# Kernel optimization log

Measured on AMD Instinct MI355X. Metric: run time of the kernel, lower is better.

## Reference

```python
import jax, jax.numpy as jnp
import numpy as np

B, C, N, H = 4, 512, 16384, 8
D = C // H
EPS = 1e-6

def setup_inputs() -> dict:
    key = jax.random.key(0)
    k1, k2, k3 = jax.random.split(key, 3)
    # xavier_normal std for Linear(C, out): sqrt(2/(fan_in+fan_out))
    std_qkv = (2.0 / (C + 3 * C)) ** 0.5
    std_proj = (2.0 / (C + C)) ** 0.5
    return {
        "x": jax.random.normal(k1, (B, C, N), dtype=jnp.float32),
        "W_qkv": jax.random.normal(k2, (C, 3 * C), dtype=jnp.float32) * std_qkv,
        "b_qkv": jnp.zeros((3 * C,), dtype=jnp.float32),
        "W_proj": jax.random.normal(k3, (C, C), dtype=jnp.float32) * std_proj,
        "b_proj": jnp.zeros((C,), dtype=jnp.float32),
    }

def _phi(x):
    return jax.nn.elu(x) + 1.0

def reference(x, W_qkv, b_qkv, W_proj, b_proj):
    # x: [B, C, N] -> [B, N, C]
    xt = jnp.swapaxes(x, 1, 2)
    qkv = xt @ W_qkv + b_qkv                      # [B, N, 3C]
    q, k, v = jnp.split(qkv, 3, axis=-1)
    # [B, N, C] -> [B, H, N, D]
    def heads(t):
        return jnp.swapaxes(t.reshape(B, N, H, D), 1, 2)
    q, k, v = heads(q), heads(k), heads(v)
    q_phi = _phi(q)                               # [B, H, N, D]
    k_phi = _phi(k)
    S = jnp.einsum('bhnd,bhne->bhde', k_phi, v)   # [B, H, D, D] KV state
    k_sum = k_phi.sum(axis=-2)                    # [B, H, D]
    num = jnp.einsum('bhnd,bhde->bhne', q_phi, S) # [B, H, N, D]
    den = jnp.einsum('bhnd,bhd->bhn', q_phi, k_sum)[..., None] + EPS
    out = num / den                               # [B, H, N, D]
    out = jnp.swapaxes(out, 1, 2).reshape(B, N, C)
    out = out @ W_proj + b_proj                   # [B, N, C]
    return jnp.swapaxes(out, 1, 2)                # [B, C, N]
```

## Files before the change

### kernel.cpp

```cpp
#include <hip/hip_runtime.h>
#include <cmath>

#define B_  4
#define C_  512
#define N_  16384
#define H_  8
#define D_  64
#define C3_ 1536
#define EPS 1e-6f

#define PADA 72
#define PADT 136
#define PADO 132

typedef __attribute__((ext_vector_type(8))) short bf16x8;
typedef __attribute__((ext_vector_type(4))) float f32x4;

__device__ __forceinline__ ushort f2bf(float f) {
    union { float f; unsigned u; } c{f};
    unsigned r = (c.u + 0x7FFF + ((c.u >> 16) & 1)) >> 16;
    return (ushort)r;
}
__device__ __forceinline__ float bf2f(ushort b) {
    union { unsigned u; float f; } c{(unsigned)b << 16};
    return c.f;
}
__device__ __forceinline__ float phi_f(float x) { return x > 0.f ? x + 1.f : __expf(x); }

__global__ __launch_bounds__(256) void k_transpose(
        const float* __restrict__ src, ushort* __restrict__ dst,
        int R, int Cc, long sStride, long dStride) {
    __shared__ ushort T[64][72];
    const long sb = (long)blockIdx.z * sStride;
    const long db = (long)blockIdx.z * dStride;
    const int c0 = blockIdx.x * 64, r0 = blockIdx.y * 64;
    const int t = threadIdx.x;
    const int ct = t & 15, rt = t >> 4;
    float4 v[4];
    #pragma unroll
    for (int k = 0; k < 4; ++k)
        v[k] = *(const float4*)(src + sb + (long)(r0 + rt * 4 + k) * Cc + c0 + ct * 4);
    #pragma unroll
    for (int j = 0; j < 4; ++j) {
        ushort pk[4];
        #pragma unroll
        for (int k = 0; k < 4; ++k) pk[k] = f2bf(((const float*)&v[k])[j]);
        *(uint2*)&T[ct * 4 + j][rt * 4] = *(uint2*)pk;
    }
    __syncthreads();
    const int c = t >> 2, rq = (t & 3) * 16;
    ushort* d = dst + db + (long)(c0 + c) * R + r0 + rq;
    *(int4*)(d)     = *(const int4*)&T[c][rq];
    *(int4*)(d + 8) = *(const int4*)&T[c][rq + 8];
}

__global__ __launch_bounds__(256) void k_kv_s(
        const ushort* __restrict__ xt, const ushort* __restrict__ Wqt,
        const float* __restrict__ bqkv, float* __restrict__ S_g,
        float* __restrict__ ksum_g) {
    const int s = blockIdx.x, h = blockIdx.y, b = blockIdx.z;
    const int tid = threadIdx.x;
    const int w = tid >> 6, ln = tid & 63, lr = ln & 15, lq = ln >> 4;
    const int bh = b * H_ + h;

    __shared__ __align__(16) char smem[128 * PADA * 2 * 2];
    ushort (*Ax)[PADA]  = (ushort(*)[PADA])smem;
    ushort (*Bw)[PADA]  = (ushort(*)[PADA])(smem + 128 * PADA * 2);
    ushort (*kvT)[PADT] = (ushort(*)[PADT])smem;
    __shared__ float biasL[128];
    __shared__ float ksRed[4][64];

    if (tid < 128) {
        int col = tid < 64 ? (512 + h * 64 + tid) : (1024 + h * 64 + (tid - 64));
        biasL[tid] = bqkv[col];
    }

    const f32x4 FZ = {0.f, 0.f, 0.f, 0.f};
    f32x4 Sacc[4] = {FZ, FZ, FZ, FZ};
    float ksp = 0.f;

    for (int it = 0; it < 8; ++it) {
        const int n0 = (s * 8 + it) * 128;
        f32x4 acc[2][8];
        #pragma unroll
        for (int mi = 0; mi < 2; mi++)
            #pragma unroll
            for (int ji = 0; ji < 8; ji++) acc[mi][ji] = FZ;

        for (int kc = 0; kc < 8; ++kc) {
            const int c0 = kc * 64;
            __syncthreads();
            {
                int row = tid >> 1, co = (tid & 1) * 32;
                const int4* srca = (const int4*)(xt + ((long)(b * N_ + n0 + row)) * C_ + c0 + co);
                int4* dsta = (int4*)&Ax[row][co];
                dsta[0] = srca[0]; dsta[1] = srca[1]; dsta[2] = srca[2]; dsta[3] = srca[3];
                int j = row;
                int wr = j < 64 ? (512 + h * 64 + j) : (1024 + h * 64 + (j - 64));
                const int4* srcb = (const int4*)(Wqt + (long)wr * C_ + c0 + co);
                int4* dstb = (int4*)&Bw[j][co];
                dstb[0] = srcb[0]; dstb[1] = srcb[1]; dstb[2] = srcb[2]; dstb[3] = srcb[3];
            }
            __syncthreads();
            #pragma unroll
            for (int ks = 0; ks < 2; ++ks) {
                bf16x8 a[2], bb[8];
                #pragma unroll
                for (int mi = 0; mi < 2; mi++)
                    a[mi] = *(const bf16x8*)&Ax[w * 32 + mi * 16 + lr][ks * 32 + lq * 8];
                #pragma unroll
                for (int ji = 0; ji < 8; ji++)
                    bb[ji] = *(const bf16x8*)&Bw[ji * 16 + lr][ks * 32 + lq * 8];
                #pragma unroll
                for (int mi = 0; mi < 2; mi++)
                    #pragma unroll
                    for (int ji = 0; ji < 8; ji++)
                        acc[mi][ji] = __builtin_amdgcn_mfma_f32_16x16x32_bf16(
                            a[mi], bb[ji], acc[mi][ji], 0, 0, 0);
            }
        }
        __syncthreads();
        #pragma unroll
        for (int mi = 0; mi < 2; mi++) {
            int nl = w * 32 + mi * 16 + lq * 4;
            #pragma unroll
            for (int ji = 0; ji < 8; ji++) {
                int j = ji * 16 + lr;
                float bs = biasL[j];
                ushort pk[4];
                #pragma unroll
                for (int r = 0; r < 4; r++) {
                    float vv = acc[mi][ji][r] + bs;
                    if (j < 64) vv = phi_f(vv);
                    pk[r] = f2bf(vv);
                }
                *(uint2*)&kvT[j][nl] = *(uint2*)pk;
            }
        }
        __syncthreads();
        #pragma unroll
        for (int ks = 0; ks < 4; ++ks) {
            bf16x8 af = *(const bf16x8*)&kvT[w * 16 + lr][ks * 32 + lq * 8];
            #pragma unroll
            for (int e = 0; e < 4; e++) {
                bf16x8 bv = *(const bf16x8*)&kvT[64 + e * 16 + lr][ks * 32 + lq * 8];
                Sacc[e] = __builtin_amdgcn_mfma_f32_16x16x32_bf16(af, bv, Sacc[e], 0, 0, 0);
            }
        }
        {
            int d = tid & 63, q = tid >> 6;
            float sum = 0.f;
            #pragma unroll
            for (int m = 0; m < 4; m++) {
                bf16x8 u = *(const bf16x8*)&kvT[d][q * 32 + m * 8];
                #pragma unroll
                for (int j = 0; j < 8; j++) sum += bf2f((ushort)u[j]);
            }
            ksp += sum;
        }
    }
    #pragma unroll
    for (int e = 0; e < 4; e++)
        #pragma unroll
        for (int r = 0; r < 4; r++)
            atomicAdd(&S_g[((long)bh * 64 + w * 16 + lq * 4 + r) * 64 + e * 16 + lr],
                      Sacc[e][r]);
    ksRed[tid >> 6][tid & 63] = ksp;
    __syncthreads();
    if (tid < 64)
        atomicAdd(&ksum_g[bh * 64 + tid],
                  ksRed[0][tid] + ksRed[1][tid] + ksRed[2][tid] + ksRed[3][tid]);
}

__global__ void k_sfin(const float* __restrict__ S_g, const float* __restrict__ ksum_g,
                       ushort* __restrict__ SbT) {
    int bh = blockIdx.x, t = threadIdx.x;
    for (int i = t; i < 5120; i += 256) {
        int e = i >> 6, d = i & 63;
        float v = (e < 64) ? S_g[(long)bh * 4096 + d * 64 + e]
                           : (e == 64 ? ksum_g[bh * 64 + d] : 0.f);
        ushort hi = f2bf(v);
        ushort lo = f2bf(v - bf2f(hi));
        SbT[(long)bh * 10240 + i] = hi;
        SbT[(long)bh * 10240 + 5120 + i] = lo;
    }
}

__global__ __launch_bounds__(256) void k_q_attn(
        const ushort* __restrict__ xt, const ushort* __restrict__ Wqt,
        const float* __restrict__ bqkv, const ushort* __restrict__ SbT,
        ushort* __restrict__ attn) {
    const int nt = blockIdx.x, h = blockIdx.y, b = blockIdx.z;
    const int n0 = nt * 128;
    const int tid = threadIdx.x;
    const int w = tid >> 6, ln = tid & 63, lr = ln & 15, lq = ln >> 4;
    const int bh = b * H_ + h;

    __shared__ __align__(16) ushort Ax[128][PADA];
    __shared__ __align__(16) ushort Bq[64][PADA];
    __shared__ __align__(16) ushort Sb[160][PADA];
    __shared__ float denL[128];

    #pragma unroll
    for (int p = 0; p < 5; ++p) {
        int r = p * 32 + (tid >> 3);
        *(int4*)&Sb[r][(tid & 7) * 8] =
            *(const int4*)(SbT + (long)bh * 10240 + r * 64 + (tid & 7) * 8);
    }

    const f32x4 FZ = {0.f, 0.f, 0.f, 0.f};
    f32x4 accq[2][4];
    #pragma unroll
    for (int mi = 0; mi < 2; mi++)
        #pragma unroll
        for (int ji = 0; ji < 4; ji++) accq[mi][ji] = FZ;

    for (int kc = 0; kc < 8; ++kc) {
        const int c0 = kc * 64;
        __syncthreads();
        {
            int row = tid >> 1, co = (tid & 1) * 32;
            const int4* srca = (const int4*)(xt + ((long)(b * N_ + n0 + row)) * C_ + c0 + co);
            int4* dsta = (int4*)&Ax[row][co];
            dsta[0] = srca[0]; dsta[1] = srca[1]; dsta[2] = srca[2]; dsta[3] = srca[3];
            if (tid < 128) {
                int j = tid >> 1;
                const int4* srcb = (const int4*)(Wqt + (long)(h * 64 + j) * C_ + c0 + co);
                int4* dstb = (int4*)&Bq[j][co];
                dstb[0] = srcb[0]; dstb[1] = srcb[1]; dstb[2] = srcb[2]; dstb[3] = srcb[3];
            }
        }
        __syncthreads();
        #pragma unroll
        for (int ks = 0; ks < 2; ++ks) {
            bf16x8 a[2], bb[4];
            #pragma unroll
            for (int mi = 0; mi < 2; mi++)
                a[mi] = *(const bf16x8*)&Ax[w * 32 + mi * 16 + lr][ks * 32 + lq * 8];
            #pragma unroll
            for (int ji = 0; ji < 4; ji++)
                bb[ji] = *(const bf16x8*)&Bq[ji * 16 + lr][ks * 32 + lq * 8];
            #pragma unroll
            for (int mi = 0; mi < 2; mi++)
                #pragma unroll
                for (int ji = 0; ji < 4; ji++)
                    accq[mi][ji] = __builtin_amdgcn_mfma_f32_16x16x32_bf16(
                        a[mi], bb[ji], accq[mi][ji], 0, 0, 0);
        }
    }
    __syncthreads();
    #pragma unroll
    for (int mi = 0; mi < 2; mi++) {
        int nl = w * 32 + mi * 16 + lq * 4;
        #pragma unroll
        for (int ji = 0; ji < 4; ji++) {
            int d = ji * 16 + lr;
            float bs = bqkv[h * 64 + d];
            #pragma unroll
            for (int r = 0; r < 4; r++)
                Ax[nl + r][d] = f2bf(phi_f(accq[mi][ji][r] + bs));
        }
    }
    __syncthreads();
    f32x4 accn[2][5];
    #pragma unroll
    for (int mi = 0; mi < 2; mi++)
        #pragma unroll
        for (int ei = 0; ei < 5; ei++) accn[mi][ei] = FZ;
    #pragma unroll
    for (int ks = 0; ks < 2; ++ks) {
        bf16x8 a[2];
        #pragma unroll
        for (int mi = 0; mi < 2; mi++)
            a[mi] = *(const bf16x8*)&Ax[w * 32 + mi * 16 + lr][ks * 32 + lq * 8];
        #pragma unroll
        for (int ei = 0; ei < 5; ei++) {
            bf16x8 bhi = *(const bf16x8*)&Sb[ei * 16 + lr][ks * 32 + lq * 8];
            bf16x8 blo = *(const bf16x8*)&Sb[80 + ei * 16 + lr][ks * 32 + lq * 8];
            #pragma unroll
            for (int mi = 0; mi < 2; mi++) {
                accn[mi][ei] = __builtin_amdgcn_mfma_f32_16x16x32_bf16(
                    a[mi], bhi, accn[mi][ei], 0, 0, 0);
                accn[mi][ei] = __builtin_amdgcn_mfma_f32_16x16x32_bf16(
                    a[mi], blo, accn[mi][ei], 0, 0, 0);
            }
        }
    }
    if (lr == 0) {
        #pragma unroll
        for (int mi = 0; mi < 2; mi++)
            #pragma unroll
            for (int r = 0; r < 4; r++)
                denL[w * 32 + mi * 16 + lq * 4 + r] = accn[mi][4][r] + EPS;
    }
    __syncthreads();
    #pragma unroll
    for (int mi = 0; mi < 2; mi++) {
        int nl = w * 32 + mi * 16 + lq * 4;
        #pragma unroll
        for (int ji = 0; ji < 4; ji++) {
            int e = ji * 16 + lr;
            #pragma unroll
            for (int r = 0; r < 4; r++)
                Ax[nl + r][e] = f2bf(accn[mi][ji][r] / denL[nl + r]);
        }
    }
    __syncthreads();
    {
        int row = tid >> 1, co = (tid & 1) * 32;
        const int4* sp = (const int4*)&Ax[row][co];
        int4* dp = (int4*)(attn + ((long)(b * N_ + n0 + row)) * C_ + h * 64 + co);
        dp[0] = sp[0]; dp[1] = sp[1]; dp[2] = sp[2]; dp[3] = sp[3];
    }
}

__global__ __launch_bounds__(256) void k_proj(
        const ushort* __restrict__ attn, const ushort* __restrict__ Wpt,
        const float* __restrict__ bproj, float* __restrict__ out) {
    const int nt = blockIdx.x, jt = blockIdx.y;
    const int tid = threadIdx.x;
    const int w = tid >> 6, ln = tid & 63, lr = ln & 15, lq = ln >> 4;
    const int b = nt >> 7;
    const int nloc = (nt & 127) * 128;

    __shared__ __align__(16) char smem[128 * PADA * 2 * 2];
    ushort (*Aa)[PADA] = (ushort(*)[PADA])smem;
    ushort (*Bw)[PADA] = (ushort(*)[PADA])(smem + 128 * PADA * 2);
    float (*outT)[PADO] = (float(*)[PADO])smem;

    const f32x4 FZ = {0.f, 0.f, 0.f, 0.f};
    f32x4 acc[2][8];
    #pragma unroll
    for (int mi = 0; mi < 2; mi++)
        #pragma unroll
        for (int ji = 0; ji < 8; ji++) acc[mi][ji] = FZ;

    for (int kc = 0; kc < 8; ++kc) {
        const int c0 = kc * 64;
        __syncthreads();
        {
            int row = tid >> 1, co = (tid & 1) * 32;
            const int4* srca = (const int4*)(attn + ((long)(nt * 128 + row)) * C_ + c0 + co);
            int4* dsta = (int4*)&Aa[row][co];
            dsta[0] = srca[0]; dsta[1] = srca[1]; dsta[2] = srca[2]; dsta[3] = srca[3];
            int j = row;
            const int4* srcb = (const int4*)(Wpt + (long)(jt * 128 + j) * C_ + c0 + co);
            int4* dstb = (int4*)&Bw[j][co];
            dstb[0] = srcb[0]; dstb[1] = srcb[1]; dstb[2] = srcb[2]; dstb[3] = srcb[3];
        }
        __syncthreads();
        #pragma unroll
        for (int ks = 0; ks < 2; ++ks) {
            bf16x8 a[2], bb[8];
            #pragma unroll
            for (int mi = 0; mi < 2; mi++)
                a[mi] = *(const bf16x8*)&Aa[w * 32 + mi * 16 + lr][ks * 32 + lq * 8];
            #pragma unroll
            for (int ji = 0; ji < 8; ji++)
                bb[ji] = *(const bf16x8*)&Bw[ji * 16 + lr][ks * 32 + lq * 8];
            #pragma unroll
            for (int mi = 0; mi < 2; mi++)
                #pragma unroll
                for (int ji = 0; ji < 8; ji++)
                    acc[mi][ji] = __builtin_amdgcn_mfma_f32_16x16x32_bf16(
                        a[mi], bb[ji], acc[mi][ji], 0, 0, 0);
        }
    }
    #pragma unroll
    for (int half = 0; half < 2; ++half) {
        __syncthreads();
        #pragma unroll
        for (int mi = 0; mi < 2; mi++) {
            int nl = w * 32 + mi * 16 + lq * 4;
            #pragma unroll
            for (int ji = 0; ji < 4; ji++) {
                int cl = ji * 16 + lr;
                float bs = bproj[jt * 128 + half * 64 + cl];
                f32x4 v = acc[mi][half * 4 + ji];
                #pragma unroll
                for (int r = 0; r < 4; r++) v[r] += bs;
                *(f32x4*)&outT[cl][nl] = v;
            }
        }
        __syncthreads();
        {
            int cl = tid >> 2, ch = (tid & 3) * 32;
            const float* sp = &outT[cl][ch];
            float* dp = out + ((long)(b * C_ + jt * 128 + half * 64 + cl)) * N_ + nloc + ch;
            #pragma unroll
            for (int k = 0; k < 8; ++k)
                ((float4*)dp)[k] = ((const float4*)sp)[k];
        }
    }
}

__global__ __launch_bounds__(256) void kernelA_fb(
        const float* __restrict__ x, const float* __restrict__ Wqkv,
        const float* __restrict__ bqkv, float* __restrict__ S_g,
        float* __restrict__ ksum_g) {
    const int h = blockIdx.x;
    const int s = blockIdx.y;
    const int b = blockIdx.z;
    const int tid = threadIdx.x;
    const int tn = tid & 15;
    const int tj = tid >> 4;
    const int td = tid & 15;
    const int te = tid >> 4;

    __shared__ float As[16][64];
    __shared__ float Bs[16][128];
    __shared__ float kphi_s[64][64];
    __shared__ float v_s[64][64];

    float acc2[4][4];
    #pragma unroll
    for (int i = 0; i < 4; i++)
        #pragma unroll
        for (int j = 0; j < 4; j++) acc2[i][j] = 0.f;
    float ksum_r = 0.f;

    float bias_j[8];
    #pragma unroll
    for (int jj = 0; jj < 8; jj++) {
        int j = tj * 8 + jj;
        int col = (j < 64) ? (512 + h * 64 + j) : (1024 + h * 64 + (j - 64));
        bias_j[jj] = bqkv[col];
    }

    for (int it = 0; it < 8; ++it) {
        const int n0 = (s * 8 + it) * 64;
        float acc[4][8];
        #pragma unroll
        for (int i = 0; i < 4; i++)
            #pragma unroll
            for (int jj = 0; jj < 8; jj++) acc[i][jj] = 0.f;

        for (int kc = 0; kc < 32; ++kc) {
            const int c0 = kc * 16;
            __syncthreads();
            {
                int r = tid >> 4, n4 = (tid & 15) * 4;
                const float* src = x + ((size_t)b * C_ + (c0 + r)) * (size_t)N_ + n0 + n4;
                *(float4*)&As[r][n4] = *(const float4*)src;
            }
            #pragma unroll
            for (int part = 0; part < 2; ++part) {
                int idx = tid + part * 256;
                int r = idx >> 5;
                int j4 = (idx & 31) * 4;
                int col = (j4 < 64) ? (512 + h * 64 + j4) : (1024 + h * 64 + (j4 - 64));
                const float* src = Wqkv + (size_t)(c0 + r) * C3_ + col;
                *(float4*)&Bs[r][j4] = *(const float4*)src;
            }
            __syncthreads();
            #pragma unroll
            for (int k = 0; k < 16; ++k) {
                float a[4], bb[8];
                *(float4*)a      = *(const float4*)&As[k][tn * 4];
                *(float4*)&bb[0] = *(const float4*)&Bs[k][tj * 8];
                *(float4*)&bb[4] = *(const float4*)&Bs[k][tj * 8 + 4];
                #pragma unroll
                for (int i = 0; i < 4; i++)
                    #pragma unroll
                    for (int jj = 0; jj < 8; jj++)
                        acc[i][jj] = fmaf(a[i], bb[jj], acc[i][jj]);
            }
        }
        __syncthreads();
        if (tj < 8) {
            #pragma unroll
            for (int i = 0; i < 4; i++) {
                int n = tn * 4 + i;
                float tmp[8];
                #pragma unroll
                for (int jj = 0; jj < 8; jj++) tmp[jj] = phi_f(acc[i][jj] + bias_j[jj]);
                *(float4*)&kphi_s[n][tj * 8]     = *(float4*)&tmp[0];
                *(float4*)&kphi_s[n][tj * 8 + 4] = *(float4*)&tmp[4];
            }
        } else {
            #pragma unroll
            for (int i = 0; i < 4; i++) {
                int n = tn * 4 + i;
                float tmp[8];
                #pragma unroll
                for (int jj = 0; jj < 8; jj++) tmp[jj] = acc[i][jj] + bias_j[jj];
                *(float4*)&v_s[n][(tj - 8) * 8]     = *(float4*)&tmp[0];
                *(float4*)&v_s[n][(tj - 8) * 8 + 4] = *(float4*)&tmp[4];
            }
        }
        __syncthreads();
        #pragma unroll 4
        for (int n = 0; n < 64; ++n) {
            float a[4], bb[4];
            *(float4*)a  = *(const float4*)&kphi_s[n][td * 4];
            *(float4*)bb = *(const float4*)&v_s[n][te * 4];
            #pragma unroll
            for (int dd = 0; dd < 4; dd++)
                #pragma unroll
                for (int ee = 0; ee < 4; ee++)
                    acc2[dd][ee] = fmaf(a[dd], bb[ee], acc2[dd][ee]);
        }
        if (tid < 64) {
            float sum = 0.f;
            #pragma unroll 8
            for (int n = 0; n < 64; ++n) sum += kphi_s[n][tid];
            ksum_r += sum;
        }
    }

    const int bh = b * H_ + h;
    #pragma unroll
    for (int dd = 0; dd < 4; dd++)
        #pragma unroll
        for (int ee = 0; ee < 4; ee++)
            atomicAdd(&S_g[((size_t)bh * 64 + td * 4 + dd) * 64 + te * 4 + ee], acc2[dd][ee]);
    if (tid < 64) atomicAdd(&ksum_g[bh * 64 + tid], ksum_r);
}

__global__ __launch_bounds__(256) void kernelB_fb(
        const float* __restrict__ x, const float* __restrict__ Wqkv,
        const float* __restrict__ bqkv, const float* __restrict__ Wproj,
        const float* __restrict__ bproj, const float* __restrict__ S_g,
        const float* __restrict__ ksum_g, float* __restrict__ out) {
    const int nt = blockIdx.x;
    const int b  = blockIdx.y;
    const int n0 = nt * 16;
    const int tid = threadIdx.x;
    const int tn = tid & 3;
    const int tj = tid >> 2;

    __shared__ float QA[512][16];
    __shared__ float As[16][16];
    __shared__ float Bs2[16][256];
    __shared__ float SB[16][64];
    __shared__ float ksumL[512];
    __shared__ float denL[16];

    ksumL[tid]       = ksum_g[(size_t)b * 512 + tid];
    ksumL[tid + 256] = ksum_g[(size_t)b * 512 + tid + 256];

    for (int half = 0; half < 2; ++half) {
        float acc[4][4];
        #pragma unroll
        for (int i = 0; i < 4; i++)
            #pragma unroll
            for (int j = 0; j < 4; j++) acc[i][j] = 0.f;

        for (int kc = 0; kc < 32; ++kc) {
            const int c0 = kc * 16;
            __syncthreads();
            {
                int r = tid >> 4, n = tid & 15;
                As[r][n] = x[((size_t)b * C_ + c0 + r) * (size_t)N_ + n0 + n];
            }
            {
                int r = tid >> 4;
                int j0 = (tid & 15) * 16;
                const float* src = Wqkv + (size_t)(c0 + r) * C3_ + half * 256 + j0;
                float4* dst = (float4*)&Bs2[r][j0];
                #pragma unroll
                for (int q4 = 0; q4 < 4; q4++) dst[q4] = ((const float4*)src)[q4];
            }
            __syncthreads();
            #pragma unroll
            for (int k = 0; k < 16; ++k) {
                float a[4], bb[4];
                *(float4*)a  = *(const float4*)&As[k][tn * 4];
                *(float4*)bb = *(const float4*)&Bs2[k][tj * 4];
                #pragma unroll
                for (int i = 0; i < 4; i++)
                    #pragma unroll
                    for (int jj = 0; jj < 4; jj++)
                        acc[i][jj] = fmaf(a[i], bb[jj], acc[i][jj]);
            }
        }
        #pragma unroll
        for (int jj = 0; jj < 4; jj++) {
            int c = half * 256 + tj * 4 + jj;
            float bq = bqkv[c];
            float tmp[4];
            #pragma unroll
            for (int i = 0; i < 4; i++) tmp[i] = phi_f(acc[i][jj] + bq);
            *(float4*)&QA[c][tn * 4] = *(float4*)tmp;
        }
    }
    __syncthreads();

    for (int h = 0; h < H_; ++h) {
        if (tid < 16) {
            float d = 0.f;
            #pragma unroll 8
            for (int dd = 0; dd < 64; ++dd)
                d = fmaf(QA[h * 64 + dd][tid], ksumL[h * 64 + dd], d);
            denL[tid] = d + EPS;
        }
        float acc4[4] = {0.f, 0.f, 0.f, 0.f};
        for (int dc = 0; dc < 4; ++dc) {
            __syncthreads();
            {
                int r = tid >> 4, e4 = (tid & 15) * 4;
                *(float4*)&SB[r][e4] =
                    *(const float4*)&S_g[(((size_t)(b * H_ + h)) * 64 + dc * 16 + r) * 64 + e4];
            }
            __syncthreads();
            #pragma unroll
            for (int k = 0; k < 16; ++k) {
                float a[4];
                *(float4*)a = *(const float4*)&QA[h * 64 + dc * 16 + k][tn * 4];
                float bb = SB[k][tj];
                #pragma unroll
                for (int i = 0; i < 4; i++) acc4[i] = fmaf(a[i], bb, acc4[i]);
            }
        }
        __syncthreads();
        {
            float tmp[4];
            #pragma unroll
            for (int i = 0; i < 4; i++) tmp[i] = acc4[i] / denL[tn * 4 + i];
            *(float4*)&QA[h * 64 + tj][tn * 4] = *(float4*)tmp;
        }
        __syncthreads();
    }

    for (int half = 0; half < 2; ++half) {
        float acc[4][4];
        #pragma unroll
        for (int i = 0; i < 4; i++)
            #pragma unroll
            for (int j = 0; j < 4; j++) acc[i][j] = 0.f;

        for (int kc = 0; kc < 32; ++kc) {
            __syncthreads();
            {
                int r = tid >> 4;
                int j0 = (tid & 15) * 16;
                const float* src = Wproj + (size_t)(kc * 16 + r) * C_ + half * 256 + j0;
                float4* dst = (float4*)&Bs2[r][j0];
                #pragma unroll
                for (int q4 = 0; q4 < 4; q4++) dst[q4] = ((const float4*)src)[q4];
            }
            __syncthreads();
            #pragma unroll
            for (int k = 0; k < 16; ++k) {
                float a[4], bb[4];
                *(float4*)a  = *(const float4*)&QA[kc * 16 + k][tn * 4];
                *(float4*)bb = *(const float4*)&Bs2[k][tj * 4];
                #pragma unroll
                for (int i = 0; i < 4; i++)
                    #pragma unroll
                    for (int jj = 0; jj < 4; jj++)
                        acc[i][jj] = fmaf(a[i], bb[jj], acc[i][jj]);
            }
        }
        #pragma unroll
        for (int jj = 0; jj < 4; jj++) {
            int c = half * 256 + tj * 4 + jj;
            float bp = bproj[c];
            float tmp[4];
            #pragma unroll
            for (int i = 0; i < 4; i++) tmp[i] = acc[i][jj] + bp;
            *(float4*)&out[((size_t)b * C_ + c) * (size_t)N_ + n0 + tn * 4] = *(float4*)tmp;
        }
    }
}

extern "C" void kernel_launch(void* const* d_in, const int* in_sizes, int n_in,
                              void* d_out, int out_size, void* d_ws, size_t ws_size,
                              hipStream_t stream) {
    const float* x     = (const float*)d_in[0];
    const float* Wqkv  = (const float*)d_in[1];
    const float* bqkv  = (const float*)d_in[2];
    const float* Wproj = (const float*)d_in[3];
    const float* bproj = (const float*)d_in[4];
    float* out = (float*)d_out;

    const size_t oS    = 0;
    const size_t oK    = oS + 524288;
    const size_t oXT   = oK + 8192;
    const size_t oWq   = oXT + 67108864;
    const size_t oWp   = oWq + 1572864;
    const size_t oSbT  = oWp + 524288;
    const size_t oAttn = oSbT + 655360;
    const size_t need  = oAttn + 67108864;

    float* S_g    = (float*)((char*)d_ws + oS);
    float* ksum_g = (float*)((char*)d_ws + oK);

    if (ws_size < need) {
        hipMemsetAsync(d_ws, 0, 532480, stream);
        kernelA_fb<<<dim3(H_, 32, B_), 256, 0, stream>>>(x, Wqkv, bqkv, S_g, ksum_g);
        kernelB_fb<<<dim3(N_ / 16, B_), 256, 0, stream>>>(x, Wqkv, bqkv, Wproj, bproj,
                                                          S_g, ksum_g, out);
        return;
    }

    ushort* xt   = (ushort*)((char*)d_ws + oXT);
    ushort* Wqt  = (ushort*)((char*)d_ws + oWq);
    ushort* Wpt  = (ushort*)((char*)d_ws + oWp);
    ushort* SbT  = (ushort*)((char*)d_ws + oSbT);
    ushort* attn = (ushort*)((char*)d_ws + oAttn);

    hipMemsetAsync(d_ws, 0, 532480, stream);
    k_transpose<<<dim3(N_ / 64, C_ / 64, B_), 256, 0, stream>>>(
        x, xt, C_, N_, (long)C_ * N_, (long)N_ * C_);
    k_transpose<<<dim3(C3_ / 64, C_ / 64, 1), 256, 0, stream>>>(
        Wqkv, Wqt, C_, C3_, 0, 0);
    k_transpose<<<dim3(C_ / 64, C_ / 64, 1), 256, 0, stream>>>(
        Wproj, Wpt, C_, C_, 0, 0);
    k_kv_s<<<dim3(16, H_, B_), 256, 0, stream>>>(xt, Wqt, bqkv, S_g, ksum_g);
    k_sfin<<<dim3(B_ * H_), 256, 0, stream>>>(S_g, ksum_g, SbT);
    k_q_attn<<<dim3(N_ / 128, H_, B_), 256, 0, stream>>>(xt, Wqt, bqkv, SbT, attn);
    k_proj<<<dim3((B_ * N_) / 128, 4), 256, 0, stream>>>(attn, Wpt, bproj, out);
}
```

Baseline: 534.4 us.

## Use direct global-to-LDS loads with XOR-swizzled layout in GEMM kernels

Replaces the register-staged global-to-shared copies in the KV-state, Q-attention and projection kernels with global_load_lds 16-byte direct loads into unpadded tiles that use an XOR swizzle to avoid bank conflicts. The k_sum reduction is computed with an MFMA against a ones vector instead of a scalar LDS reduction. The KV kernel grid is doubled with fewer iterations per block to raise parallelism. The cost is more complex swizzled indexing and more atomic traffic from the larger KV grid.

```diff
diff --git a/kernel.cpp b/kernel.cpp
--- a/kernel.cpp
+++ b/kernel.cpp
@@ -15,6 +15,15 @@
 
 typedef __attribute__((ext_vector_type(8))) short bf16x8;
 typedef __attribute__((ext_vector_type(4))) float f32x4;
+
+typedef const void __attribute__((address_space(1)))* gas_t;
+typedef void __attribute__((address_space(3)))* las_t;
+
+__device__ __forceinline__ void gld16(const void* g, void* l) {
+    __builtin_amdgcn_global_load_lds((gas_t)(unsigned long long)g,
+                                     (las_t)(unsigned)(unsigned long long)l,
+                                     16, 0, 0);
+}
 
 __device__ __forceinline__ ushort f2bf(float f) {
     union { float f; unsigned u; } c{f};
@@ -62,25 +71,40 @@
     const int tid = threadIdx.x;
     const int w = tid >> 6, ln = tid & 63, lr = ln & 15, lq = ln >> 4;
     const int bh = b * H_ + h;
-
-    __shared__ __align__(16) char smem[128 * PADA * 2 * 2];
-    ushort (*Ax)[PADA]  = (ushort(*)[PADA])smem;
-    ushort (*Bw)[PADA]  = (ushort(*)[PADA])(smem + 128 * PADA * 2);
+    const int lrow = ln >> 3;
+    const int csw  = (ln & 7) ^ lrow;
+    const int sw   = lr & 7;
+
+    __shared__ __align__(16) char smem[34816];
+    ushort* AxL = (ushort*)smem;
+    ushort* BwL = (ushort*)(smem + 16384);
     ushort (*kvT)[PADT] = (ushort(*)[PADT])smem;
     __shared__ float biasL[128];
-    __shared__ float ksRed[4][64];
 
     if (tid < 128) {
         int col = tid < 64 ? (512 + h * 64 + tid) : (1024 + h * 64 + (tid - 64));
         biasL[tid] = bqkv[col];
     }
 
+    int gA[4], gB[4];
+    #pragma unroll
+    for (int i = 0; i < 4; ++i) {
+        const int row = (w * 4 + i) * 8 + lrow;
+        gA[i] = row * C_ + csw * 8;
+        const int wr = row < 64 ? (512 + h * 64 + row) : (1024 + h * 64 + (row - 64));
+        gB[i] = wr * C_ + csw * 8;
+    }
+    const long xb = (long)b * N_ * C_;
+
     const f32x4 FZ = {0.f, 0.f, 0.f, 0.f};
     f32x4 Sacc[4] = {FZ, FZ, FZ, FZ};
-    float ksp = 0.f;
-
-    for (int it = 0; it < 8; ++it) {
-        const int n0 = (s * 8 + it) * 128;
+    f32x4 Kacc = FZ;
+    bf16x8 ONES;
+    #pragma unroll
+    for (int i = 0; i < 8; ++i) ONES[i] = (short)0x3F80;
+
+    for (int it = 0; it < 4; ++it) {
+        const ushort* xa = xt + xb + (long)((s * 4 + it) * 128) * C_;
         f32x4 acc[2][8];
         #pragma unroll
         for (int mi = 0; mi < 2; mi++)
@@ -90,27 +114,23 @@
         for (int kc = 0; kc < 8; ++kc) {
             const int c0 = kc * 64;
             __syncthreads();
-            {
-                int row = tid >> 1, co = (tid & 1) * 32;
-                const int4* srca = (const int4*)(xt + ((long)(b * N_ + n0 + row)) * C_ + c0 + co);
-                int4* dsta = (int4*)&Ax[row][co];
-                dsta[0] = srca[0]; dsta[1] = srca[1]; dsta[2] = srca[2]; dsta[3] = srca[3];
-                int j = row;
-                int wr = j < 64 ? (512 + h * 64 + j) : (1024 + h * 64 + (j - 64));
-                const int4* srcb = (const int4*)(Wqt + (long)wr * C_ + c0 + co);
-                int4* dstb = (int4*)&Bw[j][co];
-                dstb[0] = srcb[0]; dstb[1] = srcb[1]; dstb[2] = srcb[2]; dstb[3] = srcb[3];
+            #pragma unroll
+            for (int i = 0; i < 4; ++i) {
+                const int ch = w * 4 + i;
+                gld16(xa + gA[i] + c0, AxL + ch * 512);
+                gld16(Wqt + gB[i] + c0, BwL + ch * 512);
             }
             __syncthreads();
             #pragma unroll
             for (int ks = 0; ks < 2; ++ks) {
+                const int cof = ((ks * 4 + lq) ^ sw) * 8;
                 bf16x8 a[2], bb[8];
                 #pragma unroll
                 for (int mi = 0; mi < 2; mi++)
-                    a[mi] = *(const bf16x8*)&Ax[w * 32 + mi * 16 + lr][ks * 32 + lq * 8];
+                    a[mi] = *(const bf16x8*)&AxL[(w * 32 + mi * 16 + lr) * 64 + cof];
                 #pragma unroll
                 for (int ji = 0; ji < 8; ji++)
-                    bb[ji] = *(const bf16x8*)&Bw[ji * 16 + lr][ks * 32 + lq * 8];
+                    bb[ji] = *(const bf16x8*)&BwL[(ji * 16 + lr) * 64 + cof];
                 #pragma unroll
                 for (int mi = 0; mi < 2; mi++)
                     #pragma unroll
@@ -146,17 +166,7 @@
                 bf16x8 bv = *(const bf16x8*)&kvT[64 + e * 16 + lr][ks * 32 + lq * 8];
                 Sacc[e] = __builtin_amdgcn_mfma_f32_16x16x32_bf16(af, bv, Sacc[e], 0, 0, 0);
             }
-        }
-        {
-            int d = tid & 63, q = tid >> 6;
-            float sum = 0.f;
-            #pragma unroll
-            for (int m = 0; m < 4; m++) {
-                bf16x8 u = *(const bf16x8*)&kvT[d][q * 32 + m * 8];
-                #pragma unroll
-                for (int j = 0; j < 8; j++) sum += bf2f((ushort)u[j]);
-            }
-            ksp += sum;
+            Kacc = __builtin_amdgcn_mfma_f32_16x16x32_bf16(af, ONES, Kacc, 0, 0, 0);
         }
     }
     #pragma unroll
@@ -165,11 +175,11 @@
         for (int r = 0; r < 4; r++)
             atomicAdd(&S_g[((long)bh * 64 + w * 16 + lq * 4 + r) * 64 + e * 16 + lr],
                       Sacc[e][r]);
-    ksRed[tid >> 6][tid & 63] = ksp;
-    __syncthreads();
-    if (tid < 64)
-        atomicAdd(&ksum_g[bh * 64 + tid],
-                  ksRed[0][tid] + ksRed[1][tid] + ksRed[2][tid] + ksRed[3][tid]);
+    if (lr == 0) {
+        #pragma unroll
+        for (int r = 0; r < 4; r++)
+            atomicAdd(&ksum_g[bh * 64 + w * 16 + lq * 4 + r], Kacc[r]);
+    }
 }
 
 __global__ void k_sfin(const float* __restrict__ S_g, const float* __restrict__ ksum_g,
@@ -195,9 +205,10 @@
     const int tid = threadIdx.x;
     const int w = tid >> 6, ln = tid & 63, lr = ln & 15, lq = ln >> 4;
     const int bh = b * H_ + h;
-
-    __shared__ __align__(16) ushort Ax[128][PADA];
-    __shared__ __align__(16) ushort Bq[64][PADA];
+    const int lrow = ln >> 3, csw = (ln & 7) ^ lrow, sw = lr & 7;
+
+    __shared__ __align__(16) ushort AxL[128 * 64];
+    __shared__ __align__(16) ushort BqL[64 * 64];
     __shared__ __align__(16) ushort Sb[160][PADA];
     __shared__ float denL[128];
 
@@ -208,6 +219,18 @@
             *(const int4*)(SbT + (long)bh * 10240 + r * 64 + (tid & 7) * 8);
     }
 
+    int gA[4], gB[2];
+    #pragma unroll
+    for (int i = 0; i < 4; ++i) {
+        const int row = (w * 4 + i) * 8 + lrow;
+        gA[i] = (b * N_ + n0 + row) * C_ + csw * 8;
+    }
+    #pragma unroll
+    for (int i = 0; i < 2; ++i) {
+        const int j = (w * 2 + i) * 8 + lrow;
+        gB[i] = (h * 64 + j) * C_ + csw * 8;
+    }
+
     const f32x4 FZ = {0.f, 0.f, 0.f, 0.f};
     f32x4 accq[2][4];
     #pragma unroll
@@ -218,28 +241,23 @@
     for (int kc = 0; kc < 8; ++kc) {
         const int c0 = kc * 64;
         __syncthreads();
-        {
-            int row = tid >> 1, co = (tid & 1) * 32;
-            const int4* srca = (const int4*)(xt + ((long)(b * N_ + n0 + row)) * C_ + c0 + co);
-            int4* dsta = (int4*)&Ax[row][co];
-            dsta[0] = srca[0]; dsta[1] = srca[1]; dsta[2] = srca[2]; dsta[3] = srca[3];
-            if (tid < 128) {
-                int j = tid >> 1;
-                const int4* srcb = (const int4*)(Wqt + (long)(h * 64 + j) * C_ + c0 + co);
-                int4* dstb = (int4*)&Bq[j][co];
-                dstb[0] = srcb[0]; dstb[1] = srcb[1]; dstb[2] = srcb[2]; dstb[3] = srcb[3];
-            }
-        }
+        #pragma unroll
+        for (int i = 0; i < 4; ++i)
+            gld16(xt + gA[i] + c0, AxL + (w * 4 + i) * 512);
+        #pragma unroll
+        for (int i = 0; i < 2; ++i)
+            gld16(Wqt + gB[i] + c0, BqL + (w * 2 + i) * 512);
         __syncthreads();
         #pragma unroll
         for (int ks = 0; ks < 2; ++ks) {
+            const int cof = ((ks * 4 + lq) ^ sw) * 8;
             bf16x8 a[2], bb[4];
             #pragma unroll
             for (int mi = 0; mi < 2; mi++)
-                a[mi] = *(const bf16x8*)&Ax[w * 32 + mi * 16 + lr][ks * 32 + lq * 8];
+                a[mi] = *(const bf16x8*)&AxL[(w * 32 + mi * 16 + lr) * 64 + cof];
             #pragma unroll
             for (int ji = 0; ji < 4; ji++)
-                bb[ji] = *(const bf16x8*)&Bq[ji * 16 + lr][ks * 32 + lq * 8];
+                bb[ji] = *(const bf16x8*)&BqL[(ji * 16 + lr) * 64 + cof];
             #pragma unroll
             for (int mi = 0; mi < 2; mi++)
                 #pragma unroll
@@ -257,8 +275,11 @@
             int d = ji * 16 + lr;
             float bs = bqkv[h * 64 + d];
             #pragma unroll
-            for (int r = 0; r < 4; r++)
-                Ax[nl + r][d] = f2bf(phi_f(accq[mi][ji][r] + bs));
+            for (int r = 0; r < 4; r++) {
+                int row = nl + r;
+                AxL[row * 64 + ((((d >> 3) ^ (row & 7)) << 3) | (d & 7))] =
+                    f2bf(phi_f(accq[mi][ji][r] + bs));
+            }
         }
     }
     __syncthreads();
@@ -269,10 +290,11 @@
         for (int ei = 0; ei < 5; ei++) accn[mi][ei] = FZ;
     #pragma unroll
     for (int ks = 0; ks < 2; ++ks) {
+        const int cof = ((ks * 4 + lq) ^ sw) * 8;
         bf16x8 a[2];
         #pragma unroll
         for (int mi = 0; mi < 2; mi++)
-            a[mi] = *(const bf16x8*)&Ax[w * 32 + mi * 16 + lr][ks * 32 + lq * 8];
+            a[mi] = *(const bf16x8*)&AxL[(w * 32 + mi * 16 + lr) * 64 + cof];
         #pragma unroll
         for (int ei = 0; ei < 5; ei++) {
             bf16x8 bhi = *(const bf16x8*)&Sb[ei * 16 + lr][ks * 32 + lq * 8];
@@ -301,16 +323,20 @@
         for (int ji = 0; ji < 4; ji++) {
             int e = ji * 16 + lr;
             #pragma unroll
-            for (int r = 0; r < 4; r++)
-                Ax[nl + r][e] = f2bf(accn[mi][ji][r] / denL[nl + r]);
+            for (int r = 0; r < 4; r++) {
+                int row = nl + r;
+                AxL[row * 64 + ((((e >> 3) ^ (row & 7)) << 3) | (e & 7))] =
+                    f2bf(accn[mi][ji][r] / denL[row]);
+            }
         }
     }
     __syncthreads();
     {
         int row = tid >> 1, co = (tid & 1) * 32;
-        const int4* sp = (const int4*)&Ax[row][co];
         int4* dp = (int4*)(attn + ((long)(b * N_ + n0 + row)) * C_ + h * 64 + co);
-        dp[0] = sp[0]; dp[1] = sp[1]; dp[2] = sp[2]; dp[3] = sp[3];
+        #pragma unroll
+        for (int k = 0; k < 4; ++k)
+            dp[k] = *(const int4*)&AxL[row * 64 + ((((co >> 3) + k) ^ (row & 7)) << 3)];
     }
 }
 
@@ -322,11 +348,20 @@
     const int w = tid >> 6, ln = tid & 63, lr = ln & 15, lq = ln >> 4;
     const int b = nt >> 7;
     const int nloc = (nt & 127) * 128;
-
-    __shared__ __align__(16) char smem[128 * PADA * 2 * 2];
-    ushort (*Aa)[PADA] = (ushort(*)[PADA])smem;
-    ushort (*Bw)[PADA] = (ushort(*)[PADA])(smem + 128 * PADA * 2);
+    const int lrow = ln >> 3, csw = (ln & 7) ^ lrow, sw = lr & 7;
+
+    __shared__ __align__(16) char smem[36864];
+    ushort* AaL = (ushort*)smem;
+    ushort* BwL = (ushort*)(smem + 16384);
     float (*outT)[PADO] = (float(*)[PADO])smem;
+
+    int gA[4], gB[4];
+    #pragma unroll
+    for (int i = 0; i < 4; ++i) {
+        const int row = (w * 4 + i) * 8 + lrow;
+        gA[i] = (nt * 128 + row) * C_ + csw * 8;
+        gB[i] = (jt * 128 + row) * C_ + csw * 8;
+    }
 
     const f32x4 FZ = {0.f, 0.f, 0.f, 0.f};
     f32x4 acc[2][8];
@@ -338,26 +373,23 @@
     for (int kc = 0; kc < 8; ++kc) {
         const int c0 = kc * 64;
         __syncthreads();
-        {
-            int row = tid >> 1, co = (tid & 1) * 32;
-            const int4* srca = (const int4*)(attn + ((long)(nt * 128 + row)) * C_ + c0 + co);
-            int4* dsta = (int4*)&Aa[row][co];
-            dsta[0] = srca[0]; dsta[1] = srca[1]; dsta[2] = srca[2]; dsta[3] = srca[3];
-            int j = row;
-            const int4* srcb = (const int4*)(Wpt + (long)(jt * 128 + j) * C_ + c0 + co);
-            int4* dstb = (int4*)&Bw[j][co];
-            dstb[0] = srcb[0]; dstb[1] = srcb[1]; dstb[2] = srcb[2]; dstb[3] = srcb[3];
+        #pragma unroll
+        for (int i = 0; i < 4; ++i) {
+            const int ch = w * 4 + i;
+            gld16(attn + gA[i] + c0, AaL + ch * 512);
+            gld16(Wpt + gB[i] + c0, BwL + ch * 512);
         }
         __syncthreads();
         #pragma unroll
         for (int ks = 0; ks < 2; ++ks) {
+            const int cof = ((ks * 4 + lq) ^ sw) * 8;
             bf16x8 a[2], bb[8];
             #pragma unroll
             for (int mi = 0; mi < 2; mi++)
-                a[mi] = *(const bf16x8*)&Aa[w * 32 + mi * 16 + lr][ks * 32 + lq * 8];
+                a[mi] = *(const bf16x8*)&AaL[(w * 32 + mi * 16 + lr) * 64 + cof];
             #pragma unroll
             for (int ji = 0; ji < 8; ji++)
-                bb[ji] = *(const bf16x8*)&Bw[ji * 16 + lr][ks * 32 + lq * 8];
+                bb[ji] = *(const bf16x8*)&BwL[(ji * 16 + lr) * 64 + cof];
             #pragma unroll
             for (int mi = 0; mi < 2; mi++)
                 #pragma unroll
@@ -707,7 +739,7 @@
         Wqkv, Wqt, C_, C3_, 0, 0);
     k_transpose<<<dim3(C_ / 64, C_ / 64, 1), 256, 0, stream>>>(
         Wproj, Wpt, C_, C_, 0, 0);
-    k_kv_s<<<dim3(16, H_, B_), 256, 0, stream>>>(xt, Wqt, bqkv, S_g, ksum_g);
+    k_kv_s<<<dim3(32, H_, B_), 256, 0, stream>>>(xt, Wqt, bqkv, S_g, ksum_g);
     k_sfin<<<dim3(B_ * H_), 256, 0, stream>>>(S_g, ksum_g, SbT);
     k_q_attn<<<dim3(N_ / 128, H_, B_), 256, 0, stream>>>(xt, Wqt, bqkv, SbT, attn);
     k_proj<<<dim3((B_ * N_) / 128, 4), 256, 0, stream>>>(attn, Wpt, bproj, out);
```

Result: slower. 576.5 us (+7.9%).
